# Kernel optimization log

Measured on AMD Instinct MI355X. Metric: run time of the kernel, lower is better.

## Reference

```python
import jax, jax.numpy as jnp
import numpy as np


def _parallel_scan_affine(log_a, b):
    """Hillis-Steele doubling scan for h_t = a_t*h_{t-1} + b_t (h_0 = 0).

    log_a, b: (B, T, d). Operator: (la2,b2) o (la1,b1) = (la1+la2, exp(la2)*b1 + b2).
    """
    T = log_a.shape[1]
    la, bv = log_a, b
    stride = 1
    while stride < T:  # static Python loop, log2(T) rounds
        la_prev = jnp.roll(la, stride, axis=1).at[:, :stride, :].set(0.0)
        bv_prev = jnp.roll(bv, stride, axis=1).at[:, :stride, :].set(0.0)
        bv = jnp.exp(la) * bv_prev + bv
        la = la + la_prev
        stride *= 2
    return bv


def setup_inputs() -> dict:
    key = jax.random.key(0)
    kx, kwz, kwh = jax.random.split(key, 3)
    B, T, D = 4, 4096, 1024
    x = jax.random.normal(kx, (B, T, D), dtype=jnp.float32)
    # nn.Linear(D, D) weights, stored as (out, in) like torch
    Wz = jax.random.normal(kwz, (D, D), dtype=jnp.float32) * 0.02
    bz = jnp.zeros((D,), dtype=jnp.float32)
    Wh = jax.random.normal(kwh, (D, D), dtype=jnp.float32) * 0.02
    bh = jnp.zeros((D,), dtype=jnp.float32)
    return {"x": x, "Wz": Wz, "bz": bz, "Wh": Wh, "bh": bh}


def reference(x, Wz, bz, Wh, bh):
    # forward_parallel: z = sigmoid(linear_z(x)); h_tilde = linear_h(x)
    z = jax.nn.sigmoid(jnp.einsum("btd,ed->bte", x, Wz) + bz)
    h_tilde = jnp.einsum("btd,ed->bte", x, Wh) + bh
    log_a = jnp.log(1.0 - z + 1e-08)
    b = z * h_tilde
    h_out = _parallel_scan_affine(log_a, b)
    return h_out  # out_proj is Identity since d_inner == d_model
```

## Files before the change

### kernel.cpp

```cpp
#include <hip/hip_runtime.h>
#include <hip/hip_bf16.h>


typedef __bf16 bf16x8 __attribute__((ext_vector_type(8)));
typedef __bf16 bf16x4 __attribute__((ext_vector_type(4)));
typedef float  f32x4  __attribute__((ext_vector_type(4)));

#define BSZ 4
#define TSZ 4096
#define DSZ 1024
#define MSZ (BSZ*TSZ)
#define CH  32
#define NC  (TSZ/CH)

__device__ __forceinline__ void gload_lds16(const __bf16* g, __bf16* l) {
  __builtin_amdgcn_global_load_lds(
      (const __attribute__((address_space(1))) void*)g,
      (__attribute__((address_space(3))) void*)l, 16, 0, 0);
}

__global__ void convert_tile_kernel(const float* __restrict__ X,
                                    const float* __restrict__ Wz,
                                    const float* __restrict__ Wh,
                                    __bf16* __restrict__ Xc,
                                    __bf16* __restrict__ Wzc,
                                    __bf16* __restrict__ Whc)
{
  const int bx = blockIdx.x;
  const float* src; __bf16* dst; int gid;
  if (bx < 8192)      { src = X;  dst = Xc;  gid =  bx        *256 + threadIdx.x; }
  else if (bx < 8704) { src = Wz; dst = Wzc; gid = (bx - 8192)*256 + threadIdx.x; }
  else                { src = Wh; dst = Whc; gid = (bx - 8704)*256 + threadIdx.x; }
  const int l    = gid & 63;
  const int i    = (gid >> 6) & 7;
  const int kblk = (gid >> 9) & 31;
  const int rblk = gid >> 14;
  const int row  = rblk*128 + i*16 + (l & 15);
  const int col  = kblk*32 + (l >> 4)*8;
  const float* g = src + (size_t)row*DSZ + col;
  float4 v0 = *(const float4*)g;
  float4 v1 = *(const float4*)(g + 4);
  bf16x8 p;
  p[0]=(__bf16)v0.x; p[1]=(__bf16)v0.y; p[2]=(__bf16)v0.z; p[3]=(__bf16)v0.w;
  p[4]=(__bf16)v1.x; p[5]=(__bf16)v1.y; p[6]=(__bf16)v1.z; p[7]=(__bf16)v1.w;
  *(bf16x8*)(dst + (size_t)gid*8) = p;
}

__global__ __launch_bounds__(256, 2) void gemm_gate_kernel(
    const __bf16* __restrict__ Xc,  const __bf16* __restrict__ Wzc,
    const __bf16* __restrict__ Whc,
    const float* __restrict__ bz, const float* __restrict__ bh,
    __bf16* __restrict__ a_ws, float* __restrict__ b_out,
    float* __restrict__ Aprod, float* __restrict__ Bcomp)
{
  __shared__ __align__(16) __bf16 As [4096];
  __shared__ __align__(16) __bf16 Bzs[4096];
  __shared__ __align__(16) __bf16 Bhs[4096];

  const int tid  = threadIdx.x;
  const int lane = tid & 63;
  const int wv   = tid >> 6;
  const int wM   = (wv >> 1) * 64;
  const int wN   = (wv & 1) * 64;
  const int wMg  = wM >> 4;
  const int wNg  = wN >> 4;
  const int lr   = lane & 15;
  const int q    = lane >> 4;
  const int wbase = wv * 64;

  const __bf16* Xb = Xc  + (size_t)blockIdx.x * 32 * 4096;
  const __bf16* Zb = Wzc + (size_t)blockIdx.y * 32 * 4096;
  const __bf16* Hb = Whc + (size_t)blockIdx.y * 32 * 4096;

  f32x4 accz[4][4] = {};
  f32x4 acch[4][4] = {};

  for (int kblk = 0; kblk < 32; ++kblk) {
    __syncthreads();
    const size_t tb = (size_t)kblk * 4096;
    #pragma unroll
    for (int c = 0; c < 2; ++c) {
      const int eo = (c*256 + wbase + lane) * 8;
      const int lo = (c*256 + wbase) * 8;
      gload_lds16(Xb + tb + eo, As  + lo);
      gload_lds16(Zb + tb + eo, Bzs + lo);
      gload_lds16(Hb + tb + eo, Bhs + lo);
    }
    __syncthreads();

    bf16x8 af[4];
    #pragma unroll
    for (int i = 0; i < 4; ++i)
      af[i] = *(const bf16x8*)(As + (wMg + i)*512 + lane*8);
    #pragma unroll
    for (int j = 0; j < 4; ++j) {
      bf16x8 bz8 = *(const bf16x8*)(Bzs + (wNg + j)*512 + lane*8);
      bf16x8 bh8 = *(const bf16x8*)(Bhs + (wNg + j)*512 + lane*8);
      #pragma unroll
      for (int i = 0; i < 4; ++i) {
        accz[j][i] = __builtin_amdgcn_mfma_f32_16x16x32_bf16(af[i], bz8, accz[j][i], 0, 0, 0);
        acch[j][i] = __builtin_amdgcn_mfma_f32_16x16x32_bf16(af[i], bh8, acch[j][i], 0, 0, 0);
      }
    }
  }

  const int M0 = blockIdx.x * 128;
  const int N0 = blockIdx.y * 128;
  #pragma unroll
  for (int j = 0; j < 4; ++j) {
    const int e = N0 + wN + j*16 + lr;
    const float bzv = bz[e];
    const float bhv = bh[e];
    float Aseg[4], Bseg[4];
    #pragma unroll
    for (int i = 0; i < 4; ++i) {
      const int mbase = M0 + wM + i*16 + q*4;
      float A = 1.0f, Bv = 0.0f;
      #pragma unroll
      for (int r = 0; r < 4; ++r) {
        const size_t idx = (size_t)(mbase + r)*DSZ + e;
        const float pz = accz[j][i][r] + bzv;
        const float ph = acch[j][i][r] + bhv;
        const float ex = __expf(-pz);
        const float z  = 1.0f / (1.0f + ex);
        const __bf16 abf = (__bf16)fmaf(ex, z, 1e-8f);
        const float  af  = (float)abf;
        const float  bf  = z * ph;
        a_ws[idx]  = abf;
        b_out[idx] = bf;
        Bv = fmaf(af, Bv, bf);
        A *= af;
      }
      Aseg[i] = A; Bseg[i] = Bv;
    }
    #pragma unroll
    for (int i = 0; i < 4; ++i) {
      #pragma unroll
      for (int s = 16; s < 64; s <<= 1) {
        const float Ap = __shfl_up(Aseg[i], s, 64);
        const float Bp = __shfl_up(Bseg[i], s, 64);
        if (lane >= s) { Bseg[i] = fmaf(Aseg[i], Bp, Bseg[i]); Aseg[i] *= Ap; }
      }
    }
    if (q == 3) {
      #pragma unroll
      for (int c = 0; c < 2; ++c) {
        const float Ac = Aseg[2*c+1] * Aseg[2*c];
        const float Bc = fmaf(Aseg[2*c+1], Bseg[2*c], Bseg[2*c+1]);
        const int bc = (M0 + wM + c*32) >> 5;
        Aprod[(size_t)bc*DSZ + e] = Ac;
        Bcomp[(size_t)bc*DSZ + e] = Bc;
      }
    }
  }
}

__global__ void scan_pass2_kernel(const float* __restrict__ Aprod,
                                  const float* __restrict__ Bcomp,
                                  float* __restrict__ Hstart)
{
  const int lane = threadIdx.x & 63;
  const int wave = (blockIdx.x * 256 + threadIdx.x) >> 6;
  const int b = wave >> 10;
  const int d = wave & 1023;
  const size_t i0 = (size_t)(b*NC + 2*lane)*DSZ + d;
  const float A0 = Aprod[i0],       B0 = Bcomp[i0];
  const float A1 = Aprod[i0 + DSZ], B1 = Bcomp[i0 + DSZ];
  float A  = A0 * A1;
  float Bv = fmaf(A1, B0, B1);
  #pragma unroll
  for (int s = 1; s < 64; s <<= 1) {
    const float Ap = __shfl_up(A,  s, 64);
    const float Bp = __shfl_up(Bv, s, 64);
    if (lane >= s) { Bv = fmaf(A, Bp, Bv); A *= Ap; }
  }
  float Hp = __shfl_up(Bv, 1, 64);
  if (lane == 0) Hp = 0.0f;
  Hstart[i0]       = Hp;
  Hstart[i0 + DSZ] = fmaf(A0, Hp, B0);
}

__global__ void scan_pass3_kernel(const __bf16* __restrict__ a_ws,
                                  const float* __restrict__ Hstart,
                                  float* __restrict__ out)
{
  const int bc   = blockIdx.x;
  const int d0   = threadIdx.x * 4;
  const size_t base = (size_t)bc * CH * DSZ + d0;
  float4 hv = *(const float4*)(Hstart + (size_t)bc*DSZ + d0);
  float h[4] = {hv.x, hv.y, hv.z, hv.w};
  #pragma unroll 8
  for (int t = 0; t < CH; ++t) {
    bf16x4 a4 = *(const bf16x4*)(a_ws + base + (size_t)t*DSZ);
    float4 b4 = *(const float4*)(out + base + (size_t)t*DSZ);
    const float bb[4] = {b4.x, b4.y, b4.z, b4.w};
    #pragma unroll
    for (int c = 0; c < 4; ++c)
      h[c] = fmaf((float)a4[c], h[c], bb[c]);
    *(float4*)(out + base + (size_t)t*DSZ) = make_float4(h[0], h[1], h[2], h[3]);
  }
}

extern "C" void kernel_launch(void* const* d_in, const int* in_sizes, int n_in,
                              void* d_out, int out_size, void* d_ws, size_t ws_size,
                              hipStream_t stream)
{
  const float* x  = (const float*)d_in[0];
  const float* Wz = (const float*)d_in[1];
  const float* bz = (const float*)d_in[2];
  const float* Wh = (const float*)d_in[3];
  const float* bh = (const float*)d_in[4];
  float* out = (float*)d_out;

  __bf16* Xc   = (__bf16*)d_ws;
  __bf16* Wzc  = Xc  + (size_t)MSZ * DSZ;
  __bf16* Whc  = Wzc + (size_t)DSZ * DSZ;
  __bf16* a_ws = Whc + (size_t)DSZ * DSZ;
  float* Aprod  = (float*)(a_ws + (size_t)MSZ * DSZ);
  float* Bcomp  = Aprod + (size_t)BSZ*NC*DSZ;
  float* Hstart = Bcomp + (size_t)BSZ*NC*DSZ;

  convert_tile_kernel<<<9216, 256, 0, stream>>>(x, Wz, Wh, Xc, Wzc, Whc);
  gemm_gate_kernel<<<dim3(MSZ/128, DSZ/128), 256, 0, stream>>>(
      Xc, Wzc, Whc, bz, bh, a_ws, out, Aprod, Bcomp);
  scan_pass2_kernel<<<(BSZ*DSZ)/4, 256, 0, stream>>>(Aprod, Bcomp, Hstart);
  scan_pass3_kernel<<<BSZ*NC, 256, 0, stream>>>(a_ws, Hstart, out);
}
```

Measured before the change: 244.8 us.

## Coalesce bf16 convert via LDS transpose, load A fragments directly, swap grid order

```diff
diff --git a/kernel.cpp b/kernel.cpp
--- a/kernel.cpp
+++ b/kernel.cpp
@@ -19,31 +19,40 @@
       (__attribute__((address_space(3))) void*)l, 16, 0, 0);
 }
 
-__global__ void convert_tile_kernel(const float* __restrict__ X,
-                                    const float* __restrict__ Wz,
-                                    const float* __restrict__ Wh,
-                                    __bf16* __restrict__ Xc,
-                                    __bf16* __restrict__ Wzc,
-                                    __bf16* __restrict__ Whc)
-{
+__global__ __launch_bounds__(256) void convert_tile_kernel(
+    const float* __restrict__ X, const float* __restrict__ Wz,
+    const float* __restrict__ Wh,
+    __bf16* __restrict__ Xc, __bf16* __restrict__ Wzc, __bf16* __restrict__ Whc)
+{
+  __shared__ __align__(16) __bf16 T[128*40];
   const int bx = blockIdx.x;
-  const float* src; __bf16* dst; int gid;
-  if (bx < 8192)      { src = X;  dst = Xc;  gid =  bx        *256 + threadIdx.x; }
-  else if (bx < 8704) { src = Wz; dst = Wzc; gid = (bx - 8192)*256 + threadIdx.x; }
-  else                { src = Wh; dst = Whc; gid = (bx - 8704)*256 + threadIdx.x; }
-  const int l    = gid & 63;
-  const int i    = (gid >> 6) & 7;
-  const int kblk = (gid >> 9) & 31;
-  const int rblk = gid >> 14;
-  const int row  = rblk*128 + i*16 + (l & 15);
-  const int col  = kblk*32 + (l >> 4)*8;
-  const float* g = src + (size_t)row*DSZ + col;
-  float4 v0 = *(const float4*)g;
-  float4 v1 = *(const float4*)(g + 4);
-  bf16x8 p;
-  p[0]=(__bf16)v0.x; p[1]=(__bf16)v0.y; p[2]=(__bf16)v0.z; p[3]=(__bf16)v0.w;
-  p[4]=(__bf16)v1.x; p[5]=(__bf16)v1.y; p[6]=(__bf16)v1.z; p[7]=(__bf16)v1.w;
-  *(bf16x8*)(dst + (size_t)gid*8) = p;
+  const float* src; __bf16* dst; int tile;
+  if (bx < 4096)      { src = X;  dst = Xc;  tile = bx; }
+  else if (bx < 4352) { src = Wz; dst = Wzc; tile = bx - 4096; }
+  else                { src = Wh; dst = Whc; tile = bx - 4352; }
+  const int rowblk = tile >> 5;
+  const int kblk   = tile & 31;
+  const int t = threadIdx.x;
+  #pragma unroll
+  for (int rr = 0; rr < 4; ++rr) {
+    const int flat = rr*256 + t;
+    const int r    = flat >> 3;
+    const int c4   = (flat & 7) * 4;
+    float4 v = *(const float4*)(src + (size_t)(rowblk*128 + r)*DSZ + kblk*32 + c4);
+    bf16x4 p; p[0]=(__bf16)v.x; p[1]=(__bf16)v.y; p[2]=(__bf16)v.z; p[3]=(__bf16)v.w;
+    *(bf16x4*)(T + r*40 + c4) = p;
+  }
+  __syncthreads();
+  #pragma unroll
+  for (int half = 0; half < 2; ++half) {
+    const int f   = half*2048 + t*8;
+    const int i   = f >> 9;
+    const int l   = (f >> 3) & 63;
+    const int row = i*16 + (l & 15);
+    const int k   = (l >> 4) * 8;
+    bf16x8 p = *(const bf16x8*)(T + row*40 + k);
+    *(bf16x8*)(dst + (size_t)tile*4096 + f) = p;
+  }
 }
 
 __global__ __launch_bounds__(256, 2) void gemm_gate_kernel(
@@ -53,7 +62,6 @@
     __bf16* __restrict__ a_ws, float* __restrict__ b_out,
     float* __restrict__ Aprod, float* __restrict__ Bcomp)
 {
-  __shared__ __align__(16) __bf16 As [4096];
   __shared__ __align__(16) __bf16 Bzs[4096];
   __shared__ __align__(16) __bf16 Bhs[4096];
 
@@ -68,9 +76,11 @@
   const int q    = lane >> 4;
   const int wbase = wv * 64;
 
-  const __bf16* Xb = Xc  + (size_t)blockIdx.x * 32 * 4096;
-  const __bf16* Zb = Wzc + (size_t)blockIdx.y * 32 * 4096;
-  const __bf16* Hb = Whc + (size_t)blockIdx.y * 32 * 4096;
+  const int Nb = blockIdx.x;
+  const int Mb = blockIdx.y;
+  const __bf16* Xb = Xc  + (size_t)Mb * 32 * 4096;
+  const __bf16* Zb = Wzc + (size_t)Nb * 32 * 4096;
+  const __bf16* Hb = Whc + (size_t)Nb * 32 * 4096;
 
   f32x4 accz[4][4] = {};
   f32x4 acch[4][4] = {};
@@ -82,16 +92,15 @@
     for (int c = 0; c < 2; ++c) {
       const int eo = (c*256 + wbase + lane) * 8;
       const int lo = (c*256 + wbase) * 8;
-      gload_lds16(Xb + tb + eo, As  + lo);
       gload_lds16(Zb + tb + eo, Bzs + lo);
       gload_lds16(Hb + tb + eo, Bhs + lo);
     }
+    bf16x8 af[4];
+    #pragma unroll
+    for (int i = 0; i < 4; ++i)
+      af[i] = *(const bf16x8*)(Xb + tb + (size_t)(wMg + i)*512 + lane*8);
     __syncthreads();
 
-    bf16x8 af[4];
-    #pragma unroll
-    for (int i = 0; i < 4; ++i)
-      af[i] = *(const bf16x8*)(As + (wMg + i)*512 + lane*8);
     #pragma unroll
     for (int j = 0; j < 4; ++j) {
       bf16x8 bz8 = *(const bf16x8*)(Bzs + (wNg + j)*512 + lane*8);
@@ -104,8 +113,8 @@
     }
   }
 
-  const int M0 = blockIdx.x * 128;
-  const int N0 = blockIdx.y * 128;
+  const int M0 = Mb * 128;
+  const int N0 = Nb * 128;
   #pragma unroll
   for (int j = 0; j < 4; ++j) {
     const int e = N0 + wN + j*16 + lr;
@@ -124,12 +133,12 @@
         const float ex = __expf(-pz);
         const float z  = 1.0f / (1.0f + ex);
         const __bf16 abf = (__bf16)fmaf(ex, z, 1e-8f);
-        const float  af  = (float)abf;
-        const float  bf  = z * ph;
+        const float  af2 = (float)abf;
+        const float  bf2 = z * ph;
         a_ws[idx]  = abf;
-        b_out[idx] = bf;
-        Bv = fmaf(af, Bv, bf);
-        A *= af;
+        b_out[idx] = bf2;
+        Bv = fmaf(af2, Bv, bf2);
+        A *= af2;
       }
       Aseg[i] = A; Bseg[i] = Bv;
     }
@@ -220,8 +229,8 @@
   float* Bcomp  = Aprod + (size_t)BSZ*NC*DSZ;
   float* Hstart = Bcomp + (size_t)BSZ*NC*DSZ;
 
-  convert_tile_kernel<<<9216, 256, 0, stream>>>(x, Wz, Wh, Xc, Wzc, Whc);
-  gemm_gate_kernel<<<dim3(MSZ/128, DSZ/128), 256, 0, stream>>>(
+  convert_tile_kernel<<<4608, 256, 0, stream>>>(x, Wz, Wh, Xc, Wzc, Whc);
+  gemm_gate_kernel<<<dim3(8, 128), 256, 0, stream>>>(
       Xc, Wzc, Whc, bz, bh, a_ws, out, Aprod, Bcomp);
   scan_pass2_kernel<<<(BSZ*DSZ)/4, 256, 0, stream>>>(Aprod, Bcomp, Hstart);
   scan_pass3_kernel<<<BSZ*NC, 256, 0, stream>>>(a_ws, Hstart, out);
```

Measured after the change: 244.8 us. No clear change (+0.0%).
